# Kernel tuning notes

Measured on AMD Instinct MI355X. Metric: run time of the kernel, lower is better.

Reference implementation:

```python
import jax, jax.numpy as jnp
import numpy as np

EMBED_DIM = 512
PATCH = 16
QUANT_N = 1024
QUANT_DIM = 256
LN_EPS = 1e-5


def setup_inputs() -> dict:
    key = jax.random.key(0)
    k1, k2, k3, k4 = jax.random.split(key, 4)
    B, T, M = 16, 8192, 128
    fbank = jax.random.normal(k1, (B, T, M), dtype=jnp.float32)
    # xavier-normal conv weight (O,I,kH,kW), frozen in the original module
    fan = PATCH * PATCH + EMBED_DIM
    conv_w = jax.random.normal(k2, (EMBED_DIM, 1, PATCH, PATCH), dtype=jnp.float32) * np.sqrt(2.0 / fan)
    proj = jax.random.normal(k3, (EMBED_DIM, QUANT_DIM), dtype=jnp.float32) * np.sqrt(2.0 / (EMBED_DIM + QUANT_DIM))
    codebook = jax.random.normal(k4, (QUANT_N, QUANT_DIM), dtype=jnp.float32)
    return {"fbank": fbank, "conv_w": conv_w, "proj": proj, "codebook": codebook}


def _l2norm(x, eps=1e-12):
    return x / jnp.maximum(jnp.linalg.norm(x, axis=-1, keepdims=True), eps)


def reference(fbank, conv_w, proj, codebook):
    # patch embedding: Conv2d(1, D, k=16, s=16) over (B, 1, T, mel)
    x = fbank[:, None, :, :]  # B,1,T,M
    feats = jax.lax.conv_general_dilated(
        x, conv_w, window_strides=(PATCH, PATCH), padding='VALID',
        dimension_numbers=('NCHW', 'OIHW', 'NCHW'))  # B,D,T/16,M/16
    B, D, H, W = feats.shape
    feats = feats.reshape(B, D, H * W).transpose(0, 2, 1)  # B,N,D
    # LayerNorm without affine
    mu = jnp.mean(feats, axis=-1, keepdims=True)
    var = jnp.var(feats, axis=-1, keepdims=True)
    feats = (feats - mu) * jax.lax.rsqrt(var + LN_EPS)
    # random projection quantizer: l2norm(x @ P) vs l2-normalized codebook;
    # argmin euclidean distance == argmax cosine similarity for unit vectors
    p = _l2norm(jnp.einsum('bnd,dq->bnq', feats, proj))  # B,N,Q
    cb = _l2norm(codebook)                                # K,Q
    sim = jnp.einsum('bnq,kq->bnk', p, cb)                # B,N,K
    embed_ind = jnp.argmax(sim, axis=-1)                  # B,N int
    return embed_ind
```

## Files before the change

### kernel.cpp

```cpp
#include <hip/hip_runtime.h>
#include <math.h>

#define QD 256
#define QN 1024
#define TT 8192

typedef __bf16 bf16x8 __attribute__((ext_vector_type(8)));
typedef float  f32x16 __attribute__((ext_vector_type(16)));
typedef unsigned short ushort_t;
typedef unsigned short us8 __attribute__((ext_vector_type(8)));
typedef unsigned short us4 __attribute__((ext_vector_type(4)));

#define PL  0
#define MU_ 49152
#define LM_ 50176
#define T2_ 50304
#define TR_ 50432
#define CN_ 50560
#define CC_ 50688
#define SMEM_TOTAL 53760
#define CCAP 48

__device__ __forceinline__ void split3(float x, ushort_t& h, ushort_t& m, ushort_t& l) {
    unsigned int xu = __float_as_uint(x);
    h = (ushort_t)(xu >> 16);
    float hf = __uint_as_float(xu & 0xFFFF0000u);
    float r1 = x - hf;
    unsigned int r1u = __float_as_uint(r1);
    m = (ushort_t)(r1u >> 16);
    float mf = __uint_as_float(r1u & 0xFFFF0000u);
    float r2 = r1 - mf;
    l = (ushort_t)(__float_as_uint(r2) >> 16);
}
__device__ __forceinline__ f32x16 MF(bf16x8 a, bf16x8 b, f32x16 c) {
    return __builtin_amdgcn_mfma_f32_32x32x16_bf16(a, b, c, 0, 0, 0);
}
__device__ __forceinline__ unsigned fenc(float f) {
    unsigned u = __float_as_uint(f);
    return (u & 0x80000000u) ? ~u : (u | 0x80000000u);
}
__device__ __forceinline__ float fdec(unsigned u) {
    return (u & 0x80000000u) ? __uint_as_float(u ^ 0x80000000u) : __uint_as_float(~u);
}

__global__ __launch_bounds__(512) void k_pre(const float* __restrict__ convw,
                                             const float* __restrict__ proj,
                                             const float* __restrict__ cb,
                                             ushort_t* __restrict__ cbph,
                                             float* __restrict__ cbn,
                                             ushort_t* __restrict__ w2p,
                                             float* __restrict__ wsum,
                                             float* __restrict__ p1) {
    int bx = blockIdx.x, t = threadIdx.x;
    if (bx < 128) {
        int w = t >> 6, lane = t & 63;
        int c = bx*8 + w;
        float4 v = ((const float4*)(cb + (size_t)c*QD))[lane];
        float ss = v.x*v.x + v.y*v.y + v.z*v.z + v.w*v.w;
        #pragma unroll
        for (int off = 32; off > 0; off >>= 1) ss += __shfl_down(ss, off);
        ss = __shfl(ss, 0);
        float inv = 1.0f/fmaxf(sqrtf(ss), 1e-12f);
        float4 vn = make_float4(v.x*inv, v.y*inv, v.z*inv, v.w*inv);
        *(float4*)(cbn + (size_t)c*QD + 4*lane) = vn;
        int k0 = 4*lane;
        size_t base = ((size_t)(k0>>4)*32 + (c>>5))*512 + (((k0>>3)&1)*32 + (c&31))*8 + (k0&7);
        us4 hv4;
        hv4[0] = (ushort_t)(__float_as_uint(vn.x) >> 16);
        hv4[1] = (ushort_t)(__float_as_uint(vn.y) >> 16);
        hv4[2] = (ushort_t)(__float_as_uint(vn.z) >> 16);
        hv4[3] = (ushort_t)(__float_as_uint(vn.w) >> 16);
        *(us4*)(cbph + base) = hv4;
    } else if (bx < 256) {
        int col0 = (bx - 128)*2;
        int tt = t & 255, cs = t >> 8;
        int col = col0 + cs;
        __shared__ float colv[2][512];
        colv[cs][tt]       = proj[(size_t)tt*256 + col];
        colv[cs][tt + 256] = proj[(size_t)(tt+256)*256 + col];
        __syncthreads();
        float acc = 0.f;
        #pragma unroll 32
        for (int d = 0; d < 512; ++d) acc += convw[d*256 + tt] * colv[cs][d];
        ushort_t hb, mb, lb; split3(acc, hb, mb, lb);
        size_t base = ((size_t)(tt>>4)*8 + (col>>5))*512 + (((tt>>3)&1)*32 + (col&31))*8 + (tt&7);
        w2p[base] = hb;
        w2p[base + 65536] = mb;
        w2p[base + 131072] = lb;
    } else {
        if (t < 256) {
            float s = 0.f;
            #pragma unroll 32
            for (int d = 0; d < 512; ++d) s += convw[d*256 + t];
            wsum[t] = s;
        } else {
            int u = t - 256;
            float s = 0.f;
            #pragma unroll 32
            for (int d = 0; d < 512; ++d) s += proj[d*256 + u];
            p1[u] = s;
        }
    }
}

__global__ __launch_bounds__(512, 4) void k_mega(const float* __restrict__ fbank,
                                                 const ushort_t* __restrict__ w2p,
                                                 const ushort_t* __restrict__ cbph,
                                                 const float* __restrict__ cbn,
                                                 const float* __restrict__ wsum,
                                                 const float* __restrict__ p1,
                                                 int* __restrict__ out) {
    __shared__ char smem[SMEM_TOTAL];
    float*    muS   = (float*)(smem + MU_);
    float*    lnMuS = (float*)(smem + LM_);
    float*    tn2A  = (float*)(smem + T2_);
    unsigned* thrR  = (unsigned*)(smem + TR_);
    int*      cntS  = (int*)(smem + CN_);
    ushort_t* candS = (ushort_t*)(smem + CC_);

    int tid = threadIdx.x;
    int n0 = blockIdx.x * 32;
    int w = tid >> 6, lane = tid & 63;
    int n31 = lane & 31, h = lane >> 5;
    size_t loff = (size_t)lane * 16;
    const char* w2pc = (const char*)w2p;
    const char* cbhc = (const char*)cbph;

    auto loadB1 = [&](int kcv, bf16x8 (&dst)[3]) {
        #pragma unroll
        for (int q = 0; q < 3; ++q)
            dst[q] = *(const bf16x8*)(w2pc + (size_t)q*131072 + (size_t)(kcv*8 + w)*1024 + loff);
    };
    auto loadB2s = [&](int sw, int kcv, bf16x8 (&dst)[2]) {
        dst[0] = *(const bf16x8*)(cbhc + (size_t)(kcv*32 + 16*sw + w    )*1024 + loff);
        dst[1] = *(const bf16x8*)(cbhc + (size_t)(kcv*32 + 16*sw + w + 8)*1024 + loff);
    };
    auto loadA = [&](int kcv, bf16x8 (&a)[3]) {
        #pragma unroll
        for (int p = 0; p < 3; ++p)
            a[p] = *(const bf16x8*)(smem + p*16384 + kcv*1024 + loff);
    };
    auto compute6 = [&](bf16x8 (&a)[3], bf16x8 (&b)[3], f32x16& acc) {
        acc = MF(a[0], b[0], acc);
        acc = MF(a[0], b[1], acc);
        acc = MF(a[1], b[0], acc);
        acc = MF(a[1], b[1], acc);
        acc = MF(a[0], b[2], acc);
        acc = MF(a[2], b[0], acc);
    };

    float4 va[2], vb[2];
    #pragma unroll
    for (int i = 0; i < 2; ++i) {
        int id = tid + 512*i;
        int kc = id >> 6, cl = id & 63;
        int tok = cl & 31, hh2 = cl >> 5;
        int n = n0 + tok;
        int b = n >> 12, r = n & 4095, th = r >> 3, wm = r & 7;
        const float* src = fbank + ((size_t)(b*TT + th*16 + kc))*128 + wm*16 + hh2*8;
        va[i] = ((const float4*)src)[0];
        vb[i] = ((const float4*)src)[1];
    }
    int wb0 = 16*(tid >> 6) + 8*((tid >> 5) & 1);
    float4 w00 = *(const float4*)(wsum + wb0);
    float4 w01 = *(const float4*)(wsum + wb0 + 4);
    float4 w10 = *(const float4*)(wsum + wb0 + 128);
    float4 w11 = *(const float4*)(wsum + wb0 + 132);

    if (tid < 32) { tn2A[tid] = 0.f; thrR[tid] = 0u; cntS[tid] = 0; }

    float wsv[2][8];
    wsv[0][0]=w00.x; wsv[0][1]=w00.y; wsv[0][2]=w00.z; wsv[0][3]=w00.w;
    wsv[0][4]=w01.x; wsv[0][5]=w01.y; wsv[0][6]=w01.z; wsv[0][7]=w01.w;
    wsv[1][0]=w10.x; wsv[1][1]=w10.y; wsv[1][2]=w10.z; wsv[1][3]=w10.w;
    wsv[1][4]=w11.x; wsv[1][5]=w11.y; wsv[1][6]=w11.z; wsv[1][7]=w11.w;

    float mupart = 0.f;
    #pragma unroll
    for (int i = 0; i < 2; ++i) {
        int id = tid + 512*i;
        int kc = id >> 6, cl = id & 63;
        float vals[8] = {va[i].x, va[i].y, va[i].z, va[i].w, vb[i].x, vb[i].y, vb[i].z, vb[i].w};
        us8 hv, mv, lv;
        #pragma unroll
        for (int j = 0; j < 8; ++j) {
            ushort_t a_, b_, c_; split3(vals[j], a_, b_, c_);
            hv[j] = a_; mv[j] = b_; lv[j] = c_;
            mupart += vals[j] * wsv[i][j];
        }
        char* cp = smem + kc*1024 + cl*16;
        *(us8*)cp = hv;
        *(us8*)(cp + 16384) = mv;
        *(us8*)(cp + 32768) = lv;
    }

    bf16x8 bA[3], bB[3];
    loadB1(0, bA);

    float mu2 = mupart + __shfl_xor(mupart, 32);
    if (lane < 32) muS[w*32 + lane] = mu2;
    __syncthreads();

    if (tid < 32) {
        float pm = 0.f;
        #pragma unroll
        for (int s = 0; s < 8; ++s) pm += muS[s*32 + tid];
        lnMuS[tid] = pm * (1.f/512.f);
    }

    f32x16 accE, accO;
    #pragma unroll
    for (int r2 = 0; r2 < 16; ++r2) { accE[r2] = 0.f; accO[r2] = 0.f; }
    for (int kc = 0; kc < 16; kc += 2) {
        loadB1(kc + 1, bB);
        { bf16x8 a[3]; loadA(kc, a); compute6(a, bA, accE); }
        if (kc + 2 < 16) loadB1(kc + 2, bA);
        { bf16x8 a[3]; loadA(kc + 1, a); compute6(a, bB, accO); }
    }

    float p1v = p1[32*w + n31];
    bf16x8 qA[2], qB[2];
    loadB2s(0, 0, qA);

    __syncthreads();

    {
        int q = 32*w + n31;
        #pragma unroll
        for (int reg = 0; reg < 16; ++reg) {
            int tok = (reg&3) + 8*(reg>>2) + 4*h;
            float tv = (accE[reg] + accO[reg]) - lnMuS[tok]*p1v;
            *(float*)(smem + 16384 + tok*1024 + q*4) = tv;
            *(ushort_t*)(smem + (q>>4)*1024 + (((q>>3)&1)*32 + tok)*16 + (q&7)*2)
                = (ushort_t)(__float_as_uint(tv) >> 16);
            float sq2 = tv*tv;
            #pragma unroll
            for (int msk = 1; msk < 32; msk <<= 1) sq2 += __shfl_xor(sq2, msk);
            if (n31 == 0) atomicAdd(&tn2A[tok], sq2);
        }
    }
    __syncthreads();

    #pragma unroll
    for (int sw = 0; sw < 2; ++sw) {
        f32x16 s0, s1;
        #pragma unroll
        for (int r2 = 0; r2 < 16; ++r2) { s0[r2] = 0.f; s1[r2] = 0.f; }
        for (int kc = 0; kc < 16; kc += 2) {
            loadB2s(sw, kc + 1, qB);
            {
                bf16x8 ah = *(const bf16x8*)(smem + kc*1024 + loff);
                s0 = MF(ah, qA[0], s0); s1 = MF(ah, qA[1], s1);
            }
            if (kc + 2 < 16) loadB2s(sw, kc + 2, qA);
            else if (sw == 0) loadB2s(1, 0, qA);
            {
                bf16x8 ah = *(const bf16x8*)(smem + (kc+1)*1024 + loff);
                s0 = MF(ah, qB[0], s0); s1 = MF(ah, qB[1], s1);
            }
        }
        #pragma unroll
        for (int reg = 0; reg < 16; ++reg) {
            int tok = (reg&3) + 8*(reg>>2) + 4*h;
            float m = fmaxf(s0[reg], s1[reg]);
            #pragma unroll
            for (int msk = 1; msk < 32; msk <<= 1) m = fmaxf(m, __shfl_xor(m, msk));
            if (n31 == 0) atomicMax(&thrR[tok], fenc(m));
        }
        __syncthreads();
        #pragma unroll
        for (int reg = 0; reg < 16; ++reg) {
            int tok = (reg&3) + 8*(reg>>2) + 4*h;
            float th_ = fdec(thrR[tok]) - 0.04f*sqrtf(tn2A[tok]);
            if (s0[reg] >= th_) { int p = atomicAdd(&cntS[tok], 1); if (p < CCAP) candS[tok*CCAP + p] = (ushort_t)(512*sw + 32*w + n31); }
            if (s1[reg] >= th_) { int p = atomicAdd(&cntS[tok], 1); if (p < CCAP) candS[tok*CCAP + p] = (ushort_t)(512*sw + 32*(w + 8) + n31); }
        }
    }
    __syncthreads();

    int grp = lane >> 2, sub = lane & 3;
    #pragma unroll 1
    for (int tk = 0; tk < 4; ++tk) {
        int tok = 4*w + tk;
        int cnt = cntS[tok];
        bool full = (cnt > CCAP);
        int nc = full ? 1024 : cnt;
        const float4* tp4 = (const float4*)(smem + 16384 + (size_t)tok*1024);
        float bv = -3.4e38f; int bi = 0x7fffffff;
        #pragma unroll 1
        for (int base = 0; base < nc; base += 16) {
            int ci = base + grp;
            int code = 0x7fffffff;
            float part = 0.f;
            if (ci < nc) {
                code = full ? ci : (int)candS[tok*CCAP + ci];
                const float4* cp4 = (const float4*)(cbn + (size_t)code*256);
                float a0 = 0.f, a1 = 0.f, a2 = 0.f, a3 = 0.f;
                #pragma unroll
                for (int jj = 0; jj < 16; jj += 4) {
                    float4 c0 = cp4[(jj  )*4 + sub], t0 = tp4[(jj  )*4 + sub];
                    float4 c1 = cp4[(jj+1)*4 + sub], t1 = tp4[(jj+1)*4 + sub];
                    float4 c2 = cp4[(jj+2)*4 + sub], t2 = tp4[(jj+2)*4 + sub];
                    float4 c3 = cp4[(jj+3)*4 + sub], t3 = tp4[(jj+3)*4 + sub];
                    a0 += c0.x*t0.x + c0.y*t0.y + c0.z*t0.z + c0.w*t0.w;
                    a1 += c1.x*t1.x + c1.y*t1.y + c1.z*t1.z + c1.w*t1.w;
                    a2 += c2.x*t2.x + c2.y*t2.y + c2.z*t2.z + c2.w*t2.w;
                    a3 += c3.x*t3.x + c3.y*t3.y + c3.z*t3.z + c3.w*t3.w;
                }
                part = (a0 + a1) + (a2 + a3);
            }
            float d = part;
            d += __shfl_xor(d, 1);
            d += __shfl_xor(d, 2);
            if (ci >= nc) d = -3.4e38f;
            #pragma unroll
            for (int msk = 4; msk < 64; msk <<= 1) {
                float od = __shfl_xor(d, msk);
                int   oc = __shfl_xor(code, msk);
                if (od > d || (od == d && oc < code)) { d = od; code = oc; }
            }
            if (d > bv || (d == bv && code < bi)) { bv = d; bi = code; }
        }
        if (lane == 0) out[n0 + tok] = bi;
    }
}

extern "C" void kernel_launch(void* const* d_in, const int* in_sizes, int n_in,
                              void* d_out, int out_size, void* d_ws, size_t ws_size,
                              hipStream_t stream) {
    const float* fbank = (const float*)d_in[0];
    const float* convw = (const float*)d_in[1];
    const float* proj  = (const float*)d_in[2];
    const float* cbook = (const float*)d_in[3];
    int* out = (int*)d_out;

    char* ws = (char*)d_ws;
    ushort_t* cbph = (ushort_t*)ws;
    float* cbn     = (float*)(ws + 0x080000);
    ushort_t* w2p  = (ushort_t*)(ws + 0x180000);
    float* wsum    = (float*)(ws + 0x1E0000);
    float* p1      = (float*)(ws + 0x1E1000);

    hipLaunchKernelGGL(k_pre,  dim3(257),  dim3(512), 0, stream,
                       convw, proj, cbook, cbph, cbn, w2p, wsum, p1);
    hipLaunchKernelGGL(k_mega, dim3(2048), dim3(512), 0, stream,
                       fbank, w2p, cbph, cbn, wsum, p1, out);
}
```

Measured before the change: 298.8 us.

## Transpose MFMA operand order so lanes own tokens, cutting cross-lane reductions

Swaps the A/B operands of the projection and similarity MFMAs so each lane's accumulator column maps to one token instead of one output column. Per-token sum-of-squares and max reductions then happen in registers with a single cross-half shuffle, replacing 5-step shuffle trees per register and 16 atomics per lane. The fp32 projected-token rows in LDS are XOR-swizzled to avoid bank conflicts on the transposed write pattern, and the rescoring loop indexes codebook vectors with the matching swizzle. p1 is staged into shared memory because each lane now needs many p1 values.

```diff
diff --git a/kernel.cpp b/kernel.cpp
--- a/kernel.cpp
+++ b/kernel.cpp
@@ -18,7 +18,8 @@
 #define TR_ 50432
 #define CN_ 50560
 #define CC_ 50688
-#define SMEM_TOTAL 53760
+#define P1_ 53760
+#define SMEM_TOTAL 54784
 #define CCAP 48
 
 __device__ __forceinline__ void split3(float x, ushort_t& h, ushort_t& m, ushort_t& l) {
@@ -117,6 +118,7 @@
     unsigned* thrR  = (unsigned*)(smem + TR_);
     int*      cntS  = (int*)(smem + CN_);
     ushort_t* candS = (ushort_t*)(smem + CC_);
+    float*    p1S   = (float*)(smem + P1_);
 
     int tid = threadIdx.x;
     int n0 = blockIdx.x * 32;
@@ -140,13 +142,13 @@
         for (int p = 0; p < 3; ++p)
             a[p] = *(const bf16x8*)(smem + p*16384 + kcv*1024 + loff);
     };
-    auto compute6 = [&](bf16x8 (&a)[3], bf16x8 (&b)[3], f32x16& acc) {
-        acc = MF(a[0], b[0], acc);
-        acc = MF(a[0], b[1], acc);
-        acc = MF(a[1], b[0], acc);
-        acc = MF(a[1], b[1], acc);
-        acc = MF(a[0], b[2], acc);
-        acc = MF(a[2], b[0], acc);
+    auto compute6 = [&](bf16x8 (&x)[3], bf16x8 (&y)[3], f32x16& acc) {
+        acc = MF(x[0], y[0], acc);
+        acc = MF(x[0], y[1], acc);
+        acc = MF(x[1], y[0], acc);
+        acc = MF(x[1], y[1], acc);
+        acc = MF(x[0], y[2], acc);
+        acc = MF(x[2], y[0], acc);
     };
 
     float4 va[2], vb[2];
@@ -168,6 +170,7 @@
     float4 w11 = *(const float4*)(wsum + wb0 + 132);
 
     if (tid < 32) { tn2A[tid] = 0.f; thrR[tid] = 0u; cntS[tid] = 0; }
+    if (tid < 256) p1S[tid] = p1[tid];
 
     float wsv[2][8];
     wsv[0][0]=w00.x; wsv[0][1]=w00.y; wsv[0][2]=w00.z; wsv[0][3]=w00.w;
@@ -213,31 +216,33 @@
     for (int r2 = 0; r2 < 16; ++r2) { accE[r2] = 0.f; accO[r2] = 0.f; }
     for (int kc = 0; kc < 16; kc += 2) {
         loadB1(kc + 1, bB);
-        { bf16x8 a[3]; loadA(kc, a); compute6(a, bA, accE); }
+        { bf16x8 a[3]; loadA(kc, a); compute6(bA, a, accE); }
         if (kc + 2 < 16) loadB1(kc + 2, bA);
-        { bf16x8 a[3]; loadA(kc + 1, a); compute6(a, bB, accO); }
-    }
-
-    float p1v = p1[32*w + n31];
+        { bf16x8 a[3]; loadA(kc + 1, a); compute6(bB, a, accO); }
+    }
+
     bf16x8 qA[2], qB[2];
     loadB2s(0, 0, qA);
 
     __syncthreads();
 
     {
-        int q = 32*w + n31;
+        int t31 = n31;
+        float muv = lnMuS[t31];
+        int s = t31 & 7;
+        float sqacc = 0.f;
         #pragma unroll
         for (int reg = 0; reg < 16; ++reg) {
-            int tok = (reg&3) + 8*(reg>>2) + 4*h;
-            float tv = (accE[reg] + accO[reg]) - lnMuS[tok]*p1v;
-            *(float*)(smem + 16384 + tok*1024 + q*4) = tv;
-            *(ushort_t*)(smem + (q>>4)*1024 + (((q>>3)&1)*32 + tok)*16 + (q&7)*2)
+            int ql = (reg&3) + 8*(reg>>2) + 4*h;
+            int q = 32*w + ql;
+            float tv = (accE[reg] + accO[reg]) - muv * p1S[q];
+            *(float*)(smem + 16384 + t31*1024 + (((q>>2)^s)<<4) + (q&3)*4) = tv;
+            *(ushort_t*)(smem + (q>>4)*1024 + (((q>>3)&1)*32 + t31)*16 + (q&7)*2)
                 = (ushort_t)(__float_as_uint(tv) >> 16);
-            float sq2 = tv*tv;
-            #pragma unroll
-            for (int msk = 1; msk < 32; msk <<= 1) sq2 += __shfl_xor(sq2, msk);
-            if (n31 == 0) atomicAdd(&tn2A[tok], sq2);
-        }
+            sqacc += tv*tv;
+        }
+        sqacc += __shfl_xor(sqacc, 32);
+        if (h == 0) atomicAdd(&tn2A[t31], sqacc);
     }
     __syncthreads();
 
@@ -249,31 +254,33 @@
         for (int kc = 0; kc < 16; kc += 2) {
             loadB2s(sw, kc + 1, qB);
             {
-                bf16x8 ah = *(const bf16x8*)(smem + kc*1024 + loff);
-                s0 = MF(ah, qA[0], s0); s1 = MF(ah, qA[1], s1);
+                bf16x8 th = *(const bf16x8*)(smem + kc*1024 + loff);
+                s0 = MF(qA[0], th, s0); s1 = MF(qA[1], th, s1);
             }
             if (kc + 2 < 16) loadB2s(sw, kc + 2, qA);
             else if (sw == 0) loadB2s(1, 0, qA);
             {
-                bf16x8 ah = *(const bf16x8*)(smem + (kc+1)*1024 + loff);
-                s0 = MF(ah, qB[0], s0); s1 = MF(ah, qB[1], s1);
-            }
-        }
-        #pragma unroll
-        for (int reg = 0; reg < 16; ++reg) {
-            int tok = (reg&3) + 8*(reg>>2) + 4*h;
-            float m = fmaxf(s0[reg], s1[reg]);
+                bf16x8 th = *(const bf16x8*)(smem + (kc+1)*1024 + loff);
+                s0 = MF(qB[0], th, s0); s1 = MF(qB[1], th, s1);
+            }
+        }
+        {
+            float m = fmaxf(s0[0], s1[0]);
             #pragma unroll
-            for (int msk = 1; msk < 32; msk <<= 1) m = fmaxf(m, __shfl_xor(m, msk));
-            if (n31 == 0) atomicMax(&thrR[tok], fenc(m));
+            for (int r2 = 1; r2 < 16; ++r2) m = fmaxf(m, fmaxf(s0[r2], s1[r2]));
+            m = fmaxf(m, __shfl_xor(m, 32));
+            if (h == 0) atomicMax(&thrR[n31], fenc(m));
         }
         __syncthreads();
-        #pragma unroll
-        for (int reg = 0; reg < 16; ++reg) {
-            int tok = (reg&3) + 8*(reg>>2) + 4*h;
-            float th_ = fdec(thrR[tok]) - 0.04f*sqrtf(tn2A[tok]);
-            if (s0[reg] >= th_) { int p = atomicAdd(&cntS[tok], 1); if (p < CCAP) candS[tok*CCAP + p] = (ushort_t)(512*sw + 32*w + n31); }
-            if (s1[reg] >= th_) { int p = atomicAdd(&cntS[tok], 1); if (p < CCAP) candS[tok*CCAP + p] = (ushort_t)(512*sw + 32*(w + 8) + n31); }
+        {
+            float th_ = fdec(thrR[n31]) - 0.04f*sqrtf(tn2A[n31]);
+            int cb0 = 32*(16*sw + w), cb1 = 32*(16*sw + w + 8);
+            #pragma unroll
+            for (int reg = 0; reg < 16; ++reg) {
+                int cloc = (reg&3) + 8*(reg>>2) + 4*h;
+                if (s0[reg] >= th_) { int p = atomicAdd(&cntS[n31], 1); if (p < CCAP) candS[n31*CCAP + p] = (ushort_t)(cb0 + cloc); }
+                if (s1[reg] >= th_) { int p = atomicAdd(&cntS[n31], 1); if (p < CCAP) candS[n31*CCAP + p] = (ushort_t)(cb1 + cloc); }
+            }
         }
     }
     __syncthreads();
@@ -282,6 +289,7 @@
     #pragma unroll 1
     for (int tk = 0; tk < 4; ++tk) {
         int tok = 4*w + tk;
+        int s = tok & 7;
         int cnt = cntS[tok];
         bool full = (cnt > CCAP);
         int nc = full ? 1024 : cnt;
@@ -298,10 +306,12 @@
                 float a0 = 0.f, a1 = 0.f, a2 = 0.f, a3 = 0.f;
                 #pragma unroll
                 for (int jj = 0; jj < 16; jj += 4) {
-                    float4 c0 = cp4[(jj  )*4 + sub], t0 = tp4[(jj  )*4 + sub];
-                    float4 c1 = cp4[(jj+1)*4 + sub], t1 = tp4[(jj+1)*4 + sub];
-                    float4 c2 = cp4[(jj+2)*4 + sub], t2 = tp4[(jj+2)*4 + sub];
-                    float4 c3 = cp4[(jj+3)*4 + sub], t3 = tp4[(jj+3)*4 + sub];
+                    int i0 = (jj  )*4 + sub, i1 = (jj+1)*4 + sub;
+                    int i2 = (jj+2)*4 + sub, i3 = (jj+3)*4 + sub;
+                    float4 t0 = tp4[i0], c0 = cp4[i0 ^ s];
+                    float4 t1 = tp4[i1], c1 = cp4[i1 ^ s];
+                    float4 t2 = tp4[i2], c2 = cp4[i2 ^ s];
+                    float4 t3 = tp4[i3], c3 = cp4[i3 ^ s];
                     a0 += c0.x*t0.x + c0.y*t0.y + c0.z*t0.z + c0.w*t0.w;
                     a1 += c1.x*t1.x + c1.y*t1.y + c1.z*t1.z + c1.w*t1.w;
                     a2 += c2.x*t2.x + c2.y*t2.y + c2.z*t2.z + c2.w*t2.w;
```

Measured after the change: 277.5 us. -7.1%, faster.
